# Performance work log

Hardware: AMD Instinct MI355X
Metric: run time of the kernel (lower is better)

## Reference

```python
import jax, jax.numpy as jnp
import numpy as np

IN_SHAPE = (128, 128, 128)   # (d, w, h)
RES_SCALE = 1.5
SCAN_RANGE = 11.0
PROJ_NUM = 4
SPACING = np.array([1.0, 1.0, 1.0])
OUT_SHAPE = (256, 256)
BATCH = 2


def _make_grids():
    # Faithful numpy port of proj_layer._project_grid_multi (precomputed buffers).
    d, w, h = IN_SHAPE
    p = PROJ_NUM
    half = SCAN_RANGE / 2.0
    poses = np.zeros((p, 3))
    poses[:, 1] = 3.0
    poses[:, 0] = np.tan(np.linspace(-half, half, p) / 180.0 * np.pi) * 3.0
    poses[:, 2] = np.linspace(-0.2, 0.2, p)
    emi = poses * w                                  # emitter positions, (p,3)
    res_d, res_h = int(d * RES_SCALE), int(h * RES_SCALE)
    Nvec = np.array([0.0, 1.0, 0.0])
    P0 = np.linspace(0, w - 1, w)[:, None] * np.array([[0.0, 1.0, 0.0]])  # (w,3)
    lin_x = np.linspace(-res_d / 2, res_d / 2 - 1, res_d)
    lin_y = np.linspace(-res_h / 2, res_h / 2 - 1, res_h)
    gx, gy = np.meshgrid(lin_x, lin_y, indexing='ij')
    I = np.stack([gx, np.zeros_like(gx), gy], axis=-1)   # (rd,rh,3) detector plane
    I = I[None] - emi[:, None, None, :]                  # (p,rd,rh,3) ray dirs
    dxr = I / I[..., 1:2]
    In = I / np.linalg.norm(I, axis=3, keepdims=True)
    dxr = np.linalg.norm(dxr * SPACING[None, None, None, :], axis=3)  # (p,rd,rh) step length
    inv_IN = 1.0 / (In @ Nvec)                           # (p,rd,rh)
    PN = (P0[None] - emi[:, None, :]) @ Nvec             # (p,w)
    T = inv_IN[..., None] * PN[:, None, None, :]         # (p,rd,rh,w) ray params
    grid = In[..., None, :] * T[..., None] + emi[:, None, None, None, :]  # (p,rd,rh,w,3)
    gn = np.empty_like(grid)
    gn[..., 0] = grid[..., 0] / d * 2.0
    gn[..., 1] = grid[..., 1] / w * 2.0 - 1.0
    gn[..., 2] = grid[..., 2] / h * 2.0
    gn = gn[..., ::-1]  # torch.flip(grid, [4]) -> grid_sample (x,y,z) order
    return np.ascontiguousarray(gn).astype(np.float32), dxr.astype(np.float32)


def setup_inputs() -> dict:
    key = jax.random.key(0)
    x = jax.random.normal(key, (BATCH,) + IN_SHAPE, dtype=jnp.float32)
    g, dxr = _make_grids()
    return {"x": x, "grids": jnp.asarray(g), "dx": jnp.asarray(dxr)}


def _trilinear_gather(vol, coords):
    # vol: (b, D, H, W); coords: (N,3) normalized [-1,1], (x,y,z) -> (W,H,D)
    # F.grid_sample(mode='bilinear', padding_mode='zeros', align_corners=True)
    b, D, H, W = vol.shape
    ix = (coords[:, 0] + 1.0) * 0.5 * (W - 1)
    iy = (coords[:, 1] + 1.0) * 0.5 * (H - 1)
    iz = (coords[:, 2] + 1.0) * 0.5 * (D - 1)
    x0, y0, z0 = jnp.floor(ix), jnp.floor(iy), jnp.floor(iz)
    fx, fy, fz = ix - x0, iy - y0, iz - z0
    volf = vol.reshape(b, -1)
    out = jnp.zeros((b, coords.shape[0]), vol.dtype)
    for dz in (0, 1):
        wz = fz if dz else 1.0 - fz
        zi = z0 + dz
        for dy in (0, 1):
            wy = fy if dy else 1.0 - fy
            yi = y0 + dy
            for dxx in (0, 1):
                wx = fx if dxx else 1.0 - fx
                xi = x0 + dxx
                valid = ((xi >= 0) & (xi <= W - 1) & (yi >= 0) & (yi <= H - 1)
                         & (zi >= 0) & (zi <= D - 1))
                idx = ((jnp.clip(zi, 0, D - 1).astype(jnp.int32) * H
                        + jnp.clip(yi, 0, H - 1).astype(jnp.int32)) * W
                       + jnp.clip(xi, 0, W - 1).astype(jnp.int32))
                wgt = jnp.where(valid, wx * wy * wz, 0.0)
                out = out + volf[:, idx] * wgt[None, :]
    return out


def _nearest_resize(t, out_hw):
    # F.interpolate(mode='nearest'): src = floor(dst * in / out)
    b, c, H, W = t.shape
    oh, ow = out_hw
    hi = jnp.minimum((jnp.arange(oh) * H) // oh, H - 1)
    wi = jnp.minimum((jnp.arange(ow) * W) // ow, W - 1)
    return t[:, :, hi][:, :, :, wi]


def reference(x, grids, dx):
    p, rd, rh, w = grids.shape[:4]
    b = x.shape[0]
    coords = grids.reshape(-1, 3)                       # (p*rd*rh*w, 3)
    samples = _trilinear_gather(x, coords).reshape(b, p, rd, rh, w)
    x_proj = samples.sum(axis=4) * dx[None]             # ray-sum projection
    return _nearest_resize(x_proj, OUT_SHAPE)
```

## Files before the change

### kernel.cpp

```cpp
#include <hip/hip_runtime.h>
#include <hip/hip_bf16.h>

#define PNUM 4
#define RD   192
#define RH   192
#define OHH  256
#define OWW  256
#define NB   2
#define ROWS (PNUM * RD * RH)
#define VOL  (128 * 128 * 128)
#define NRDP (PNUM * RD)

typedef float        vf4 __attribute__((ext_vector_type(4)));
typedef float        vf2 __attribute__((ext_vector_type(2)));

__device__ __forceinline__ int swz(int e) { return e ^ ((e >> 4) & 7); }


__global__ __launch_bounds__(256) void ray_setup_kernel(
    const float* __restrict__ grids,
    float* __restrict__ rayp,
    float* __restrict__ zp)
{
    const int ray = (int)(blockIdx.x * 256 + threadIdx.x);
    const float* g = grids + (size_t)ray * 384;
    const vf4 L0 = *(const vf4*)g;
    const vf4 L1 = *(const vf4*)(g + 192);
    vf2 r;
    r.x = (L0.x + 1.f) * 63.5f;
    r.y = (L1.x - L0.x) * 0.9921875f;
    *(vf2*)(rayp + (size_t)ray * 2) = r;
    if ((ray % RH) == 0) {
        vf2 z;
        z.x = (L0.z + 1.f) * 63.5f;
        z.y = (L1.z - L0.z) * 0.9921875f;
        *(vf2*)(zp + (size_t)(ray / RH) * 2) = z;
    }
}

__global__ __launch_bounds__(256) void proj_kernel(
    const float* __restrict__ x,
    const float* __restrict__ rayp,
    const float* __restrict__ zp,
    float* __restrict__ part)
{
    __shared__ __align__(16) vf2 lds[2][4][128];

    const int orig = (int)blockIdx.x;
    const int bsw  = (orig & 7) * (3072 / 8) + (orig >> 3);
    const int rdp  = bsw % NRDP;
    const int q    = bsw / NRDP;
    const int wq   = q * 32;

    const int tid  = (int)threadIdx.x;
    const int wv   = tid >> 6;
    const int lane = tid & 63;

    const vf2 zv = *(const vf2*)(zp + (size_t)rdp * 2);

    const int  ray  = rdp * RH + wv * 64 + lane;
    const bool comp = (wv < 3);
    vf2 xp = {0.f, 0.f};
    if (comp) xp = *(const vf2*)(rayp + (size_t)ray * 2);

    vf2 r00, r01, r10, r11, s00, s01, s10, s11;
    float WY0s = 0.f, WZ0s = 0.f, WZ1s = 0.f;

    auto stage_load = [&](int wb) {
        const int   w  = wb + wv;
        const float iz = fmaf((float)w, zv.y, zv.x);
        const float zf = floorf(iz);
        const float fz = iz - zf;
        const int   zb = (int)zf;
        const int zi0 = min(max(zb,     0), 127);
        const int zi1 = min(max(zb + 1, 0), 127);
        WZ0s = (zb >= 0  && zb <= 127) ? (1.f - fz) : 0.f;
        WZ1s = (zb >= -1 && zb <= 126) ? fz         : 0.f;
        WY0s = (float)w * 0.0078125f;
        const int y0 = (w > 0) ? (w - 1) : 0;
        const int y1 = w;
        const int j  = 2 * lane;
        const float* base0 = x + ((size_t)zi0 * 128 + y0) * 128 + j;
        const float* base1 = x + ((size_t)zi0 * 128 + y1) * 128 + j;
        const float* base2 = x + ((size_t)zi1 * 128 + y0) * 128 + j;
        const float* base3 = x + ((size_t)zi1 * 128 + y1) * 128 + j;
        r00 = *(const vf2*)base0;         r01 = *(const vf2*)base1;
        r10 = *(const vf2*)base2;         r11 = *(const vf2*)base3;
        s00 = *(const vf2*)(base0 + VOL); s01 = *(const vf2*)(base1 + VOL);
        s10 = *(const vf2*)(base2 + VOL); s11 = *(const vf2*)(base3 + VOL);
    };
    auto stage_write = [&](int buf) {
        const float WY1s = 1.f - WY0s;
        const vf2 a0 = WY0s * r00 + WY1s * r01;
        const vf2 b0 = WY0s * r10 + WY1s * r11;
        const vf2 c0 = WZ0s * a0 + WZ1s * b0;
        const vf2 a1 = WY0s * s00 + WY1s * s01;
        const vf2 b1 = WY0s * s10 + WY1s * s11;
        const vf2 c1 = WZ0s * a1 + WZ1s * b1;
        vf2 e0; e0.x = c0.x; e0.y = c1.x;
        vf2 e1; e1.x = c0.y; e1.y = c1.y;
        lds[buf][wv][swz(2 * lane)]     = e0;
        lds[buf][wv][swz(2 * lane + 1)] = e1;
    };

    stage_load(wq);
    stage_write(0);
    __syncthreads();

    vf2 acc = {0.f, 0.f};

    for (int c = 0; c < 8; ++c) {
        const int  buf = c & 1;
        const int  wb  = wq + c * 4;
        const bool pre = (c < 7);

        if (pre) stage_load(wb + 4);

        if (comp) {
#pragma unroll
            for (int wu = 0; wu < 4; ++wu) {
                const float wf = (float)(wb + wu);
                const float ix = fmaf(wf, xp.y, xp.x);
                const float xf = floorf(ix);
                const float fx = ix - xf;
                const int   xb = (int)xf;
                const int   xl = min(max(xb, 0), 126);
                const bool  inx = (xb >= 0) && (xb <= 126);
                const float WL = inx ? (1.f - fx) : ((xb == -1)  ? fx         : 0.f);
                const float WR = inx ? fx         : ((xb == 127) ? (1.f - fx) : 0.f);

                const vf2 c0 = lds[buf][wu][swz(xl)];
                const vf2 c1 = lds[buf][wu][swz(xl + 1)];
                acc = acc + WL * c0 + WR * c1;
            }
        }

        if (pre) stage_write(buf ^ 1);
        __syncthreads();
    }

    if (comp) {
        part[((size_t)q * NB + 0) * ROWS + ray] = acc.x;
        part[((size_t)q * NB + 1) * ROWS + ray] = acc.y;
    }
}


__global__ __launch_bounds__(256) void proj_rays_fb_kernel(
    const float* __restrict__ x,
    const float* __restrict__ grids,
    float* __restrict__ part)
{
    const int tid  = (int)(blockIdx.x * blockDim.x + threadIdx.x);
    const int wave = tid >> 6;
    const int lane = tid & 63;
    const int wcc  = wave & 3;
    const int rr   = wave >> 2;
    const int ray  = rr * 64 + lane;

    const float* g  = grids + (size_t)ray * 384 + wcc * 96;
    const float* v0 = x;
    const float* v1 = x + VOL;

    float s0 = 0.f, s1 = 0.f;
    for (int w0 = 0; w0 < 32; w0 += 16) {
        const vf4* gc = (const vf4*)(g + w0 * 3);
        float cf[48];
#pragma unroll
        for (int i = 0; i < 12; ++i) {
            const vf4 t = gc[i];
            cf[4*i+0] = t.x; cf[4*i+1] = t.y; cf[4*i+2] = t.z; cf[4*i+3] = t.w;
        }
#pragma unroll
        for (int w = 0; w < 16; ++w) {
            const float ix = (cf[3*w+0] + 1.f) * 63.5f;
            const float iy = (cf[3*w+1] + 1.f) * 63.5f;
            const float iz = (cf[3*w+2] + 1.f) * 63.5f;
            const float x0f = floorf(ix), y0f = floorf(iy), z0f = floorf(iz);
            const float fxx = ix - x0f, fyy = iy - y0f, fzz = iz - z0f;
            const float wx0 = (x0f >= 0.f && x0f <= 127.f) ? (1.f-fxx) : 0.f;
            const float wx1 = (x0f+1.f >= 0.f && x0f+1.f <= 127.f) ? fxx : 0.f;
            const float wy0 = (y0f >= 0.f && y0f <= 127.f) ? (1.f-fyy) : 0.f;
            const float wy1 = (y0f+1.f >= 0.f && y0f+1.f <= 127.f) ? fyy : 0.f;
            const float wz0 = (z0f >= 0.f && z0f <= 127.f) ? (1.f-fzz) : 0.f;
            const float wz1 = (z0f+1.f >= 0.f && z0f+1.f <= 127.f) ? fzz : 0.f;
            const int xi0 = (int)fminf(fmaxf(x0f,0.f),127.f);
            const int xi1 = (int)fminf(fmaxf(x0f+1.f,0.f),127.f);
            const int yi0 = (int)fminf(fmaxf(y0f,0.f),127.f);
            const int yi1 = (int)fminf(fmaxf(y0f+1.f,0.f),127.f);
            const int zi0 = (int)fminf(fmaxf(z0f,0.f),127.f);
            const int zi1 = (int)fminf(fmaxf(z0f+1.f,0.f),127.f);
            const int b00 = (zi0*128+yi0)*128, b01 = (zi0*128+yi1)*128;
            const int b10 = (zi1*128+yi0)*128, b11 = (zi1*128+yi1)*128;
            const float w000 = wz0*wy0*wx0, w001 = wz0*wy0*wx1;
            const float w010 = wz0*wy1*wx0, w011 = wz0*wy1*wx1;
            const float w100 = wz1*wy0*wx0, w101 = wz1*wy0*wx1;
            const float w110 = wz1*wy1*wx0, w111 = wz1*wy1*wx1;
            s0 += w000*v0[b00+xi0] + w001*v0[b00+xi1] + w010*v0[b01+xi0] + w011*v0[b01+xi1]
                + w100*v0[b10+xi0] + w101*v0[b10+xi1] + w110*v0[b11+xi0] + w111*v0[b11+xi1];
            s1 += w000*v1[b00+xi0] + w001*v1[b00+xi1] + w010*v1[b01+xi0] + w011*v1[b01+xi1]
                + w100*v1[b10+xi0] + w101*v1[b10+xi1] + w110*v1[b11+xi0] + w111*v1[b11+xi1];
        }
    }
    part[((size_t)wcc * NB + 0) * ROWS + ray] = s0;
    part[((size_t)wcc * NB + 1) * ROWS + ray] = s1;
}


__global__ __launch_bounds__(256) void resize_reduce_kernel(
    const float* __restrict__ part,
    const float* __restrict__ dx,
    float* __restrict__ out,
    int wsplit)
{
    const int idx = (int)(blockIdx.x * blockDim.x + threadIdx.x);
    const int ow = idx & (OWW - 1);
    const int oh = (idx >> 8) & (OHH - 1);
    const int bp = idx >> 16;
    const int b  = bp >> 2;
    const int p  = bp & 3;
    const int hi = (oh * 3) >> 2;
    const int wi = (ow * 3) >> 2;
    const int ray = (p * RD + hi) * RH + wi;

    float s = 0.f;
    for (int wcc = 0; wcc < wsplit; ++wcc)
        s += part[((size_t)wcc * NB + b) * ROWS + ray];
    out[idx] = s * dx[ray];
}

extern "C" void kernel_launch(void* const* d_in, const int* in_sizes, int n_in,
                              void* d_out, int out_size, void* d_ws, size_t ws_size,
                              hipStream_t stream) {
    const float* x     = (const float*)d_in[0];
    const float* grids = (const float*)d_in[1];
    const float* dx    = (const float*)d_in[2];
    float* out = (float*)d_out;
    char*  ws  = (char*)d_ws;

    const size_t RAYP_B = (size_t)ROWS * 2 * 4;
    const size_t ZP_B   = (size_t)NRDP * 2 * 4;
    const size_t PART_B = (size_t)4 * NB * ROWS * 4;
    const size_t NEED   = RAYP_B + ZP_B + PART_B;

    if (ws_size >= NEED) {
        float* rayp = (float*)ws;
        float* zp   = (float*)(ws + RAYP_B);
        float* part = (float*)(ws + RAYP_B + ZP_B);

        ray_setup_kernel<<<ROWS / 256, 256, 0, stream>>>(grids, rayp, zp);
        proj_kernel     <<<4 * NRDP, 256, 0, stream>>>(x, rayp, zp, part);
        resize_reduce_kernel<<<(NB * PNUM * OHH * OWW) / 256, 256, 0, stream>>>(part, dx, out, 4);
    } else {
        float* part = (float*)ws;
        proj_rays_fb_kernel<<<ROWS * 4 / 256, 256, 0, stream>>>(x, grids, part);
        resize_reduce_kernel<<<(NB * PNUM * OHH * OWW) / 256, 256, 0, stream>>>(part, dx, out, 4);
    }
}
```

Measured before the change: 306.7 us.

## Fuse ray setup into projection kernel and deepen LDS pipeline to three buffers

New measurement: 303.4 us. Within noise of the previous version (-1.1%).

```diff
diff --git a/kernel.cpp b/kernel.cpp
--- a/kernel.cpp
+++ b/kernel.cpp
@@ -1,5 +1,4 @@
 #include <hip/hip_runtime.h>
-#include <hip/hip_bf16.h>
 
 #define PNUM 4
 #define RD   192
@@ -11,40 +10,23 @@
 #define VOL  (128 * 128 * 128)
 #define NRDP (PNUM * RD)
 
-typedef float        vf4 __attribute__((ext_vector_type(4)));
-typedef float        vf2 __attribute__((ext_vector_type(2)));
+typedef float vf4 __attribute__((ext_vector_type(4)));
+typedef float vf2 __attribute__((ext_vector_type(2)));
 
 __device__ __forceinline__ int swz(int e) { return e ^ ((e >> 4) & 7); }
 
 
-__global__ __launch_bounds__(256) void ray_setup_kernel(
-    const float* __restrict__ grids,
-    float* __restrict__ rayp,
-    float* __restrict__ zp)
-{
-    const int ray = (int)(blockIdx.x * 256 + threadIdx.x);
-    const float* g = grids + (size_t)ray * 384;
-    const vf4 L0 = *(const vf4*)g;
-    const vf4 L1 = *(const vf4*)(g + 192);
-    vf2 r;
-    r.x = (L0.x + 1.f) * 63.5f;
-    r.y = (L1.x - L0.x) * 0.9921875f;
-    *(vf2*)(rayp + (size_t)ray * 2) = r;
-    if ((ray % RH) == 0) {
-        vf2 z;
-        z.x = (L0.z + 1.f) * 63.5f;
-        z.y = (L1.z - L0.z) * 0.9921875f;
-        *(vf2*)(zp + (size_t)(ray / RH) * 2) = z;
-    }
-}
+struct Stage {
+    vf2 r00, r01, r10, r11, s00, s01, s10, s11;
+    float WY0, WZ0, WZ1;
+};
 
 __global__ __launch_bounds__(256) void proj_kernel(
     const float* __restrict__ x,
-    const float* __restrict__ rayp,
-    const float* __restrict__ zp,
+    const float* __restrict__ grids,
     float* __restrict__ part)
 {
-    __shared__ __align__(16) vf2 lds[2][4][128];
+    __shared__ __align__(16) vf2 lds[3][4][128];
 
     const int orig = (int)blockIdx.x;
     const int bsw  = (orig & 7) * (3072 / 8) + (orig >> 3);
@@ -56,17 +38,23 @@
     const int wv   = tid >> 6;
     const int lane = tid & 63;
 
-    const vf2 zv = *(const vf2*)(zp + (size_t)rdp * 2);
+    const float* g0 = grids + (size_t)(rdp * RH) * 384;
+    const float gz0 = g0[2], gz64 = g0[2 + 192];
+    vf2 zv;
+    zv.x = (gz0 + 1.f) * 63.5f;
+    zv.y = (gz64 - gz0) * 0.9921875f;
 
     const int  ray  = rdp * RH + wv * 64 + lane;
     const bool comp = (wv < 3);
     vf2 xp = {0.f, 0.f};
-    if (comp) xp = *(const vf2*)(rayp + (size_t)ray * 2);
-
-    vf2 r00, r01, r10, r11, s00, s01, s10, s11;
-    float WY0s = 0.f, WZ0s = 0.f, WZ1s = 0.f;
-
-    auto stage_load = [&](int wb) {
+    if (comp) {
+        const float* gr = grids + (size_t)ray * 384;
+        const float gx0 = gr[0], gx64 = gr[192];
+        xp.x = (gx0 + 1.f) * 63.5f;
+        xp.y = (gx64 - gx0) * 0.9921875f;
+    }
+
+    auto stage_load = [&](int wb, Stage& S) {
         const int   w  = wb + wv;
         const float iz = fmaf((float)w, zv.y, zv.x);
         const float zf = floorf(iz);
@@ -74,49 +62,52 @@
         const int   zb = (int)zf;
         const int zi0 = min(max(zb,     0), 127);
         const int zi1 = min(max(zb + 1, 0), 127);
-        WZ0s = (zb >= 0  && zb <= 127) ? (1.f - fz) : 0.f;
-        WZ1s = (zb >= -1 && zb <= 126) ? fz         : 0.f;
-        WY0s = (float)w * 0.0078125f;
+        S.WZ0 = (zb >= 0  && zb <= 127) ? (1.f - fz) : 0.f;
+        S.WZ1 = (zb >= -1 && zb <= 126) ? fz         : 0.f;
+        S.WY0 = (float)w * 0.0078125f;
         const int y0 = (w > 0) ? (w - 1) : 0;
         const int y1 = w;
         const int j  = 2 * lane;
-        const float* base0 = x + ((size_t)zi0 * 128 + y0) * 128 + j;
-        const float* base1 = x + ((size_t)zi0 * 128 + y1) * 128 + j;
-        const float* base2 = x + ((size_t)zi1 * 128 + y0) * 128 + j;
-        const float* base3 = x + ((size_t)zi1 * 128 + y1) * 128 + j;
-        r00 = *(const vf2*)base0;         r01 = *(const vf2*)base1;
-        r10 = *(const vf2*)base2;         r11 = *(const vf2*)base3;
-        s00 = *(const vf2*)(base0 + VOL); s01 = *(const vf2*)(base1 + VOL);
-        s10 = *(const vf2*)(base2 + VOL); s11 = *(const vf2*)(base3 + VOL);
+        const float* b0 = x + ((size_t)zi0 * 128 + y0) * 128 + j;
+        const float* b1 = x + ((size_t)zi0 * 128 + y1) * 128 + j;
+        const float* b2 = x + ((size_t)zi1 * 128 + y0) * 128 + j;
+        const float* b3 = x + ((size_t)zi1 * 128 + y1) * 128 + j;
+        S.r00 = *(const vf2*)b0;         S.r01 = *(const vf2*)b1;
+        S.r10 = *(const vf2*)b2;         S.r11 = *(const vf2*)b3;
+        S.s00 = *(const vf2*)(b0 + VOL); S.s01 = *(const vf2*)(b1 + VOL);
+        S.s10 = *(const vf2*)(b2 + VOL); S.s11 = *(const vf2*)(b3 + VOL);
     };
-    auto stage_write = [&](int buf) {
-        const float WY1s = 1.f - WY0s;
-        const vf2 a0 = WY0s * r00 + WY1s * r01;
-        const vf2 b0 = WY0s * r10 + WY1s * r11;
-        const vf2 c0 = WZ0s * a0 + WZ1s * b0;
-        const vf2 a1 = WY0s * s00 + WY1s * s01;
-        const vf2 b1 = WY0s * s10 + WY1s * s11;
-        const vf2 c1 = WZ0s * a1 + WZ1s * b1;
+    auto stage_write = [&](int buf, const Stage& S) {
+        const float WY1 = 1.f - S.WY0;
+        const vf2 a0 = S.WY0 * S.r00 + WY1 * S.r01;
+        const vf2 b0 = S.WY0 * S.r10 + WY1 * S.r11;
+        const vf2 c0 = S.WZ0 * a0 + S.WZ1 * b0;
+        const vf2 a1 = S.WY0 * S.s00 + WY1 * S.s01;
+        const vf2 b1 = S.WY0 * S.s10 + WY1 * S.s11;
+        const vf2 c1 = S.WZ0 * a1 + S.WZ1 * b1;
         vf2 e0; e0.x = c0.x; e0.y = c1.x;
         vf2 e1; e1.x = c0.y; e1.y = c1.y;
         lds[buf][wv][swz(2 * lane)]     = e0;
         lds[buf][wv][swz(2 * lane + 1)] = e1;
     };
 
-    stage_load(wq);
-    stage_write(0);
+    Stage SA, SB;
+    vf2 acc = {0.f, 0.f};
+
+    stage_load(wq + 0, SA);
+    stage_write(0, SA);
+    stage_load(wq + 4, SA);
     __syncthreads();
 
-    vf2 acc = {0.f, 0.f};
-
+#pragma unroll
     for (int c = 0; c < 8; ++c) {
-        const int  buf = c & 1;
-        const int  wb  = wq + c * 4;
-        const bool pre = (c < 7);
-
-        if (pre) stage_load(wb + 4);
+        if (c + 2 < 8) {
+            if ((c & 1) == 0) stage_load(wq + (c + 2) * 4, SB);
+            else              stage_load(wq + (c + 2) * 4, SA);
+        }
 
         if (comp) {
+            const int wb = wq + c * 4;
 #pragma unroll
             for (int wu = 0; wu < 4; ++wu) {
                 const float wf = (float)(wb + wu);
@@ -129,13 +120,17 @@
                 const float WL = inx ? (1.f - fx) : ((xb == -1)  ? fx         : 0.f);
                 const float WR = inx ? fx         : ((xb == 127) ? (1.f - fx) : 0.f);
 
-                const vf2 c0 = lds[buf][wu][swz(xl)];
-                const vf2 c1 = lds[buf][wu][swz(xl + 1)];
+                const vf2 c0 = lds[c % 3][wu][swz(xl)];
+                const vf2 c1 = lds[c % 3][wu][swz(xl + 1)];
                 acc = acc + WL * c0 + WR * c1;
             }
         }
 
-        if (pre) stage_write(buf ^ 1);
+        if (c + 1 < 8) {
+            if ((c & 1) == 0) stage_write((c + 1) % 3, SA);
+            else              stage_write((c + 1) % 3, SB);
+        }
+
         __syncthreads();
     }
 
@@ -210,8 +205,7 @@
 __global__ __launch_bounds__(256) void resize_reduce_kernel(
     const float* __restrict__ part,
     const float* __restrict__ dx,
-    float* __restrict__ out,
-    int wsplit)
+    float* __restrict__ out)
 {
     const int idx = (int)(blockIdx.x * blockDim.x + threadIdx.x);
     const int ow = idx & (OWW - 1);
@@ -224,7 +218,8 @@
     const int ray = (p * RD + hi) * RH + wi;
 
     float s = 0.f;
-    for (int wcc = 0; wcc < wsplit; ++wcc)
+#pragma unroll
+    for (int wcc = 0; wcc < 4; ++wcc)
         s += part[((size_t)wcc * NB + b) * ROWS + ray];
     out[idx] = s * dx[ray];
 }
@@ -235,25 +230,15 @@
     const float* x     = (const float*)d_in[0];
     const float* grids = (const float*)d_in[1];
     const float* dx    = (const float*)d_in[2];
-    float* out = (float*)d_out;
-    char*  ws  = (char*)d_ws;
-
-    const size_t RAYP_B = (size_t)ROWS * 2 * 4;
-    const size_t ZP_B   = (size_t)NRDP * 2 * 4;
-    const size_t PART_B = (size_t)4 * NB * ROWS * 4;
-    const size_t NEED   = RAYP_B + ZP_B + PART_B;
+    float* out  = (float*)d_out;
+    float* part = (float*)d_ws;
+
+    const size_t NEED = (size_t)4 * NB * ROWS * 4;
 
     if (ws_size >= NEED) {
-        float* rayp = (float*)ws;
-        float* zp   = (float*)(ws + RAYP_B);
-        float* part = (float*)(ws + RAYP_B + ZP_B);
-
-        ray_setup_kernel<<<ROWS / 256, 256, 0, stream>>>(grids, rayp, zp);
-        proj_kernel     <<<4 * NRDP, 256, 0, stream>>>(x, rayp, zp, part);
-        resize_reduce_kernel<<<(NB * PNUM * OHH * OWW) / 256, 256, 0, stream>>>(part, dx, out, 4);
+        proj_kernel<<<4 * NRDP, 256, 0, stream>>>(x, grids, part);
     } else {
-        float* part = (float*)ws;
         proj_rays_fb_kernel<<<ROWS * 4 / 256, 256, 0, stream>>>(x, grids, part);
-        resize_reduce_kernel<<<(NB * PNUM * OHH * OWW) / 256, 256, 0, stream>>>(part, dx, out, 4);
-    }
-}
+    }
+    resize_reduce_kernel<<<(NB * PNUM * OHH * OWW) / 256, 256, 0, stream>>>(part, dx, out);
+}
```
